# Optimization experiments

Measured on AMD Instinct MI355X. Metric: run time of the kernel, lower is better.

## Reference

```python
import jax, jax.numpy as jnp
import numpy as np

E = 256   # embed_dim
H = 8     # num_heads
D = E // H  # head_dim = 32
L = 1024  # seq len (Q_len == K_len == V_len)


def setup_inputs() -> dict:
    key = jax.random.key(0)
    ks = jax.random.split(key, 10)
    f = lambda k, s: jax.random.normal(k, s, dtype=jnp.float32)
    return {
        "V": f(ks[0], (L, E)),
        "K": f(ks[1], (L, E)),
        "Q": f(ks[2], (L, E)),
        # genomic-style coordinates, strictly positive
        "position": jax.random.uniform(ks[3], (L,), dtype=jnp.float32) * 1e5,
        "Wq": f(ks[4], (E, E)) * 0.02,
        "Wk": f(ks[5], (E, E)) * 0.02,
        "Wv": f(ks[6], (E, E)) * 0.02,
        "Wr": f(ks[7], (E, 1)) * 0.02,   # K_relative_linear weight [out=E, in=1]
        "Wo": f(ks[8], (E, E)) * 0.02,
        "bo": jnp.zeros((E,), jnp.float32),
    }


def reference(V, K, Q, position, Wq, Wk, Wv, Wr, Wo, bo):
    Lq = Q.shape[0]
    # projections (nn.Linear: x @ W.T), split into heads -> (L, H, D)
    q = (Q @ Wq.T).reshape(Lq, H, D)
    k = (K @ Wk.T).reshape(Lq, H, D)
    v = (V @ Wv.T).reshape(Lq, H, D)

    # relative position scalar per (q, k) pair: log(|p_q - p_k| + 1)
    rel = jnp.log(jnp.abs(position[:, None] - position[None, :]) + 1.0)  # (L, L)

    # K_relative_linear maps scalar rel -> (H, D); the einsum
    # 'nqhd,nhqjd->nhqj' then factorizes exactly as:
    #   sum_d Q[q,h,d] * rel[q,j] * Wr[h,d] = (Q . Wr)[h,q] * rel[q,j]
    # so we avoid materializing the (H, L, L, D) tensor while computing
    # mathematically identical results.
    Wr_h = Wr[:, 0].reshape(H, D)                    # (H, D)
    coeff = jnp.einsum('qhd,hd->hq', q, Wr_h)        # (H, L)

    energy = jnp.einsum('qhd,khd->hqk', q, k)        # (H, L, L)
    energy = energy + coeff[:, :, None] * rel[None, :, :]

    attn = jax.nn.softmax(energy / np.float32(E) ** 0.5, axis=2)
    out = jnp.einsum('hqk,khd->qhd', attn, v).reshape(Lq, E)
    out = out @ Wo.T + bo
    return out
```

## Files before the change

### kernel.cpp

```cpp
#include <hip/hip_runtime.h>
#include <math.h>

#define EDIM 256
#define LDIM 1024
#define HDIM 8
#define DDIM 32

typedef __attribute__((ext_vector_type(8))) short short8;
typedef __attribute__((ext_vector_type(4))) float f32x4;

__device__ inline unsigned short bf16h(float x) {
    unsigned u = __float_as_uint(x);
    return (unsigned short)((u + 0x7fff + ((u >> 16) & 1)) >> 16);
}
__device__ inline float bf16tof(unsigned short h) {
    return __uint_as_float(((unsigned)h) << 16);
}
__device__ inline float exp2fast(float x) {
    float r; asm volatile("v_exp_f32 %0, %1" : "=v"(r) : "v"(x)); return r;
}
__device__ inline float log2fast(float x) {
    float r; asm volatile("v_log_f32 %0, %1" : "=v"(r) : "v"(x)); return r;
}

#define SC2 0.09016843880556021f

__global__ __launch_bounds__(256) void proj_kernel(
    const float* __restrict__ Q, const float* __restrict__ Km, const float* __restrict__ V,
    const float* __restrict__ Wq, const float* __restrict__ Wk, const float* __restrict__ Wv,
    const float* __restrict__ Wr, const float* __restrict__ Wo,
    short* __restrict__ qThi, short* __restrict__ qTlo,
    short* __restrict__ kThi, short* __restrict__ kTlo,
    short* __restrict__ vThi, short* __restrict__ vTlo,
    float* __restrict__ coeff, short* __restrict__ Wohi, short* __restrict__ Wolo)
{
    const int z = blockIdx.z;
    const int tid = threadIdx.x;

    if (z == 3) {
        const int idx = ((blockIdx.y * 32 + blockIdx.x) << 8) + tid;
        const float w = Wo[idx];
        const unsigned short hh = bf16h(w);
        Wohi[idx] = (short)hh;
        Wolo[idx] = (short)bf16h(w - bf16tof(hh));
        return;
    }

    const float* __restrict__ X = (z == 0) ? Q : (z == 1) ? Km : V;
    const float* __restrict__ W = (z == 0) ? Wq : (z == 1) ? Wk : Wv;
    short* __restrict__ dhi     = (z == 0) ? qThi : (z == 1) ? kThi : vThi;
    short* __restrict__ dlo     = (z == 0) ? qTlo : (z == 1) ? kTlo : vTlo;

    const int n0 = blockIdx.x * 32;
    const int o0 = blockIdx.y * 32;
    const int wave = tid >> 6, lane = tid & 63;
    const int n = lane & 15, quad = lane >> 4;
    const int rh = wave & 1, oh = wave >> 1;

    const int s    = tid >> 7;
    const int r    = (tid >> 2) & 31;
    const int qd   = tid & 3;
    const int half = r >> 4;
    const int fl8  = ((r & 15) | (qd << 4)) * 8;

    __shared__ short Xhi[2][2][512], Xlo[2][2][512];
    __shared__ short Whi[2][2][512], Wlo[2][2][512];
    __shared__ float cpart[2][2][16];

    const float* xp = X + (n0 + r) * EDIM + s * 32 + qd * 8;
    const float* wp = W + (o0 + r) * EDIM + s * 32 + qd * 8;

    float4 xa0 = *(const float4*)xp, xa1 = *(const float4*)(xp + 4);
    float4 wa0 = *(const float4*)wp, wa1 = *(const float4*)(wp + 4);

    f32x4 acc = {0.f, 0.f, 0.f, 0.f};

    for (int kb = 0; kb < EDIM; kb += 64) {
        __syncthreads();
        {
            float xv[8] = {xa0.x,xa0.y,xa0.z,xa0.w, xa1.x,xa1.y,xa1.z,xa1.w};
            float wv[8] = {wa0.x,wa0.y,wa0.z,wa0.w, wa1.x,wa1.y,wa1.z,wa1.w};
            short8 xh, xl, wh, wl;
            #pragma unroll
            for (int j = 0; j < 8; ++j) {
                unsigned short xhh = bf16h(xv[j]);
                unsigned short whh = bf16h(wv[j]);
                xh[j] = (short)xhh; xl[j] = (short)bf16h(xv[j] - bf16tof(xhh));
                wh[j] = (short)whh; wl[j] = (short)bf16h(wv[j] - bf16tof(whh));
            }
            *(short8*)&Xhi[s][half][fl8] = xh;
            *(short8*)&Xlo[s][half][fl8] = xl;
            *(short8*)&Whi[s][half][fl8] = wh;
            *(short8*)&Wlo[s][half][fl8] = wl;
        }
        float4 xn0, xn1, wn0, wn1;
        if (kb + 64 < EDIM) {
            xn0 = *(const float4*)(xp + kb + 64); xn1 = *(const float4*)(xp + kb + 68);
            wn0 = *(const float4*)(wp + kb + 64); wn1 = *(const float4*)(wp + kb + 68);
        }
        __syncthreads();
        #pragma unroll
        for (int ss = 0; ss < 2; ++ss) {
            short8 ah = *(const short8*)&Xhi[ss][rh][lane*8];
            short8 al = *(const short8*)&Xlo[ss][rh][lane*8];
            short8 bh = *(const short8*)&Whi[ss][oh][lane*8];
            short8 bl = *(const short8*)&Wlo[ss][oh][lane*8];
            acc = __builtin_amdgcn_mfma_f32_16x16x32_bf16(al, bh, acc, 0, 0, 0);
            acc = __builtin_amdgcn_mfma_f32_16x16x32_bf16(ah, bl, acc, 0, 0, 0);
            acc = __builtin_amdgcn_mfma_f32_16x16x32_bf16(ah, bh, acc, 0, 0, 0);
        }
        xa0 = xn0; xa1 = xn1; wa0 = wn0; wa1 = wn1;
    }

    const int h  = o0 >> 5;
    const int og = oh * 16 + n;
    #pragma unroll
    for (int i = 0; i < 4; ++i) {
        const int row = rh * 16 + 4 * quad + i;
        const unsigned short hh = bf16h(acc[i]);
        dhi[(h * LDIM + n0 + row) * DDIM + og] = (short)hh;
        dlo[(h * LDIM + n0 + row) * DDIM + og] = (short)bf16h(acc[i] - bf16tof(hh));
    }

    if (z == 0) {
        const float wr = Wr[o0 + og];
        #pragma unroll
        for (int i = 0; i < 4; ++i) {
            float c = acc[i] * wr;
            c += __shfl_xor(c, 1, 64);
            c += __shfl_xor(c, 2, 64);
            c += __shfl_xor(c, 4, 64);
            c += __shfl_xor(c, 8, 64);
            if (n == 0) cpart[rh][oh][4*quad + i] = c;
        }
        __syncthreads();
        if (tid < 32)
            coeff[h * LDIM + n0 + tid] = cpart[tid >> 4][0][tid & 15]
                                       + cpart[tid >> 4][1][tid & 15];
    }
}

__global__ __launch_bounds__(256, 4) void attn_kernel(
    const short* __restrict__ qThi, const short* __restrict__ qTlo,
    const short* __restrict__ kThi, const short* __restrict__ kTlo,
    const short* __restrict__ vThi, const short* __restrict__ vTlo,
    const float* __restrict__ coeff, const float* __restrict__ pos,
    float* __restrict__ Op, float* __restrict__ Mp, float* __restrict__ Lp, int nkt)
{
    const int h   = blockIdx.y;
    const int q0  = blockIdx.x * 64;
    const int p   = blockIdx.z;
    const int kt0 = p * nkt * 64;
    const int tid  = threadIdx.x;
    const int wave = tid >> 6;
    const int lane = tid & 63;
    const int n    = lane & 15;
    const int quad = lane >> 4;
    const int qs0  = wave * 16;

    __shared__ __align__(16) short khi[4*64*8];
    __shared__ __align__(16) short klo[4*64*8];
    __shared__ __align__(16) short vs_hi[32][72];
    __shared__ __align__(16) short vs_lo[32][72];
    __shared__ __align__(16) short pa_hi[64][72];
    __shared__ __align__(16) short pa_lo[64][72];
    __shared__ float pk[64];

    const short8 qhi = *(const short8*)(qThi + (h*LDIM + q0 + qs0 + n) * DDIM + quad*8);
    const short8 qlo = *(const short8*)(qTlo + (h*LDIM + q0 + qs0 + n) * DDIM + quad*8);

    float pq[4], cq[4];
    #pragma unroll
    for (int i = 0; i < 4; ++i) {
        const int r = q0 + qs0 + 4*quad + i;
        pq[i] = pos[r];
        cq[i] = coeff[h*LDIM + r] * 0.0625f;
    }

    float m[4], l[4];
    #pragma unroll
    for (int i = 0; i < 4; ++i) { m[i] = -INFINITY; l[i] = 0.f; }

    f32x4 of0 = {0.f,0.f,0.f,0.f}, of1 = {0.f,0.f,0.f,0.f};

    const int cS = tid >> 2;
    const int dq = tid & 3;
    const int lane2 = (cS & 15) | (dq << 4);
    const int gS = cS >> 4;

    short8 khi_c, klo_c, vhi_c, vlo_c; float pkc = 0.f;
    {
        const int off = (h*LDIM + kt0 + cS) * DDIM + dq*8;
        khi_c = *(const short8*)(kThi + off);
        klo_c = *(const short8*)(kTlo + off);
        vhi_c = *(const short8*)(vThi + off);
        vlo_c = *(const short8*)(vTlo + off);
        if (tid < 64) pkc = pos[kt0 + tid];
    }

    for (int t = 0; t < nkt; ++t) {
        __syncthreads();

        *((short8*)&khi[(gS*64 + lane2)*8]) = khi_c;
        *((short8*)&klo[(gS*64 + lane2)*8]) = klo_c;
        #pragma unroll
        for (int j = 0; j < 8; ++j) {
            vs_hi[dq*8 + j][cS] = vhi_c[j];
            vs_lo[dq*8 + j][cS] = vlo_c[j];
        }
        if (tid < 64) pk[tid] = pkc;

        short8 khi_n, klo_n, vhi_n, vlo_n; float pkn = 0.f;
        if (t + 1 < nkt) {
            const int off = (h*LDIM + kt0 + (t+1)*64 + cS) * DDIM + dq*8;
            khi_n = *(const short8*)(kThi + off);
            klo_n = *(const short8*)(kTlo + off);
            vhi_n = *(const short8*)(vThi + off);
            vlo_n = *(const short8*)(vTlo + off);
            if (tid < 64) pkn = pos[kt0 + (t+1)*64 + tid];
        }
        __syncthreads();

        f32x4 Sf[4];
        #pragma unroll
        for (int t4 = 0; t4 < 4; ++t4) {
            short8 bhi = *((const short8*)&khi[(t4*64 + lane)*8]);
            short8 blo = *((const short8*)&klo[(t4*64 + lane)*8]);
            f32x4 acc = {0.f, 0.f, 0.f, 0.f};
            acc = __builtin_amdgcn_mfma_f32_16x16x32_bf16(qlo, bhi, acc, 0, 0, 0);
            acc = __builtin_amdgcn_mfma_f32_16x16x32_bf16(qhi, blo, acc, 0, 0, 0);
            acc = __builtin_amdgcn_mfma_f32_16x16x32_bf16(qhi, bhi, acc, 0, 0, 0);
            Sf[t4] = acc;
        }

        float ev[4][4];
        float rmax[4] = {-INFINITY, -INFINITY, -INFINITY, -INFINITY};
        #pragma unroll
        for (int t4 = 0; t4 < 4; ++t4) {
            const float pkt = pk[16*t4 + n];
            #pragma unroll
            for (int i = 0; i < 4; ++i) {
                float s = fmaf(Sf[t4][i], SC2, cq[i] * log2fast(fabsf(pq[i] - pkt) + 1.f));
                ev[t4][i] = s;
                rmax[i] = fmaxf(rmax[i], s);
            }
        }
        #pragma unroll
        for (int off = 1; off < 16; off <<= 1)
            #pragma unroll
            for (int i = 0; i < 4; ++i)
                rmax[i] = fmaxf(rmax[i], __shfl_xor(rmax[i], off, 64));

        float al[4], rsum[4];
        #pragma unroll
        for (int i = 0; i < 4; ++i) {
            const float mn = fmaxf(m[i], rmax[i]);
            al[i] = exp2fast(m[i] - mn);
            m[i] = mn;
            rsum[i] = 0.f;
        }
        #pragma unroll
        for (int t4 = 0; t4 < 4; ++t4)
            #pragma unroll
            for (int i = 0; i < 4; ++i) {
                float e = exp2fast(ev[t4][i] - m[i]);
                rsum[i] += e;
                unsigned u = __float_as_uint(e);
                pa_hi[qs0 + 4*quad + i][16*t4 + n] = (short)(u >> 16);
                float r = e - __uint_as_float(u & 0xffff0000u);
                pa_lo[qs0 + 4*quad + i][16*t4 + n] = (short)bf16h(r);
            }
        #pragma unroll
        for (int off = 1; off < 16; off <<= 1)
            #pragma unroll
            for (int i = 0; i < 4; ++i)
                rsum[i] += __shfl_xor(rsum[i], off, 64);
        #pragma unroll
        for (int i = 0; i < 4; ++i) l[i] = l[i]*al[i] + rsum[i];

        #pragma unroll
        for (int i = 0; i < 4; ++i) { of0[i] *= al[i]; of1[i] *= al[i]; }

        #pragma unroll
        for (int ch = 0; ch < 2; ++ch) {
            short8 phi = *(const short8*)&pa_hi[qs0 + n][ch*32 + quad*8];
            short8 plo = *(const short8*)&pa_lo[qs0 + n][ch*32 + quad*8];
            #pragma unroll
            for (int dt = 0; dt < 2; ++dt) {
                short8 vh8 = *(const short8*)&vs_hi[dt*16 + n][ch*32 + quad*8];
                short8 vl8 = *(const short8*)&vs_lo[dt*16 + n][ch*32 + quad*8];
                f32x4& of = dt ? of1 : of0;
                of = __builtin_amdgcn_mfma_f32_16x16x32_bf16(plo, vh8, of, 0, 0, 0);
                of = __builtin_amdgcn_mfma_f32_16x16x32_bf16(phi, vl8, of, 0, 0, 0);
                of = __builtin_amdgcn_mfma_f32_16x16x32_bf16(phi, vh8, of, 0, 0, 0);
            }
        }

        khi_c = khi_n; klo_c = klo_n; vhi_c = vhi_n; vlo_c = vlo_n; pkc = pkn;
    }

    const int ph = p * HDIM + h;
    {
        const size_t base = ((size_t)ph * LDIM + q0 + qs0) * DDIM;
        #pragma unroll
        for (int i = 0; i < 4; ++i) {
            Op[base + (size_t)(4*quad + i)*DDIM + n]      = of0[i];
            Op[base + (size_t)(4*quad + i)*DDIM + 16 + n] = of1[i];
        }
    }
    if (n == 0) {
        #pragma unroll
        for (int i = 0; i < 4; ++i) {
            const int r = q0 + qs0 + 4*quad + i;
            Mp[ph*LDIM + r] = m[i];
            Lp[ph*LDIM + r] = l[i];
        }
    }
}

__global__ __launch_bounds__(256) void finale_kernel(
    const float* __restrict__ Op, const float* __restrict__ Mp, const float* __restrict__ Lp,
    const short* __restrict__ Wohi, const short* __restrict__ Wolo,
    const float* __restrict__ bo, int P, float* __restrict__ out)
{
    const int n0 = blockIdx.x * 8;
    const int tid = threadIdx.x;

    __shared__ __align__(16) short Ahi[8][264], Alo[8][264];

    {
        const int r  = tid >> 5;
        const int c8 = (tid & 31) * 8;
        const int hh = c8 >> 5;
        const int d  = c8 & 31;
        float mv[8], lv[8];
        float mx = -INFINITY;
        #pragma unroll
        for (int p = 0; p < 8; ++p) if (p < P) {
            mv[p] = Mp[(p*HDIM + hh)*LDIM + n0 + r];
            lv[p] = Lp[(p*HDIM + hh)*LDIM + n0 + r];
            mx = fmaxf(mx, mv[p]);
        }
        float s = 0.f;
        #pragma unroll
        for (int p = 0; p < 8; ++p) if (p < P) {
            float a = exp2fast(mv[p] - mx);
            mv[p] = a;
            s += a * lv[p];
        }
        const float inv = 1.f / s;
        float a[8] = {0.f,0.f,0.f,0.f,0.f,0.f,0.f,0.f};
        #pragma unroll
        for (int p = 0; p < 8; ++p) if (p < P) {
            const float sp = mv[p] * inv;
            const float* op = Op + ((size_t)(p*HDIM + hh)*LDIM + n0 + r)*DDIM + d;
            float4 x0 = *(const float4*)op;
            float4 x1 = *(const float4*)(op + 4);
            a[0] += sp*x0.x; a[1] += sp*x0.y; a[2] += sp*x0.z; a[3] += sp*x0.w;
            a[4] += sp*x1.x; a[5] += sp*x1.y; a[6] += sp*x1.z; a[7] += sp*x1.w;
        }
        short8 ah8, al8;
        #pragma unroll
        for (int j = 0; j < 8; ++j) {
            const unsigned short hhh = bf16h(a[j]);
            ah8[j] = (short)hhh;
            al8[j] = (short)bf16h(a[j] - bf16tof(hhh));
        }
        *(short8*)&Ahi[r][c8] = ah8;
        *(short8*)&Alo[r][c8] = al8;
    }
    __syncthreads();

    const int wave = tid >> 6, lane = tid & 63;
    const int n = lane & 15, quad = lane >> 4;
    const int ow = wave * 64;
    const int rA = n & 7;

    f32x4 acc[4];
    #pragma unroll
    for (int cf = 0; cf < 4; ++cf) { acc[cf][0]=0.f; acc[cf][1]=0.f; acc[cf][2]=0.f; acc[cf][3]=0.f; }

    #pragma unroll
    for (int kk = 0; kk < 8; ++kk) {
        short8 ah = *(const short8*)&Ahi[rA][kk*32 + quad*8];
        short8 al = *(const short8*)&Alo[rA][kk*32 + quad*8];
        #pragma unroll
        for (int cf = 0; cf < 4; ++cf) {
            const int o = ow + cf*16 + n;
            short8 bh = *(const short8*)(Wohi + o*EDIM + kk*32 + quad*8);
            short8 bl = *(const short8*)(Wolo + o*EDIM + kk*32 + quad*8);
            acc[cf] = __builtin_amdgcn_mfma_f32_16x16x32_bf16(al, bh, acc[cf], 0, 0, 0);
            acc[cf] = __builtin_amdgcn_mfma_f32_16x16x32_bf16(ah, bl, acc[cf], 0, 0, 0);
            acc[cf] = __builtin_amdgcn_mfma_f32_16x16x32_bf16(ah, bh, acc[cf], 0, 0, 0);
        }
    }

    if (quad < 2) {
        #pragma unroll
        for (int cf = 0; cf < 4; ++cf) {
            const int o = ow + cf*16 + n;
            const float b = bo[o];
            #pragma unroll
            for (int i = 0; i < 4; ++i) {
                const int row = n0 + 4*quad + i;
                out[row*EDIM + o] = acc[cf][i] + b;
            }
        }
    }
}

extern "C" void kernel_launch(void* const* d_in, const int* in_sizes, int n_in,
                              void* d_out, int out_size, void* d_ws, size_t ws_size,
                              hipStream_t stream) {
    const float* V   = (const float*)d_in[0];
    const float* K   = (const float*)d_in[1];
    const float* Q   = (const float*)d_in[2];
    const float* pos = (const float*)d_in[3];
    const float* Wq  = (const float*)d_in[4];
    const float* Wk  = (const float*)d_in[5];
    const float* Wv  = (const float*)d_in[6];
    const float* Wr  = (const float*)d_in[7];
    const float* Wo  = (const float*)d_in[8];
    const float* bo  = (const float*)d_in[9];
    float* out = (float*)d_out;
    char* base = (char*)d_ws;

    auto need = [](int P) -> size_t { return 3440640 + (size_t)P * 1114112; };
    int P = 2;
    if (ws_size >= need(8)) P = 8;
    else if (ws_size >= need(4)) P = 4;

    short* qThi  = (short*)(base);
    short* qTlo  = (short*)(base + 524288);
    short* kThi  = (short*)(base + 1048576);
    short* kTlo  = (short*)(base + 1572864);
    short* vThi  = (short*)(base + 2097152);
    short* vTlo  = (short*)(base + 2621440);
    float* coeff = (float*)(base + 3145728);
    short* Wohi  = (short*)(base + 3178496);
    short* Wolo  = (short*)(base + 3309568);
    float* Op    = (float*)(base + 3440640);
    float* Mp    = Op + (size_t)P * 262144;
    float* Lp    = Mp + (size_t)P * 8192;

    proj_kernel  <<<dim3(32, 8, 4), 256, 0, stream>>>(Q, K, V, Wq, Wk, Wv, Wr, Wo,
                                                      qThi, qTlo, kThi, kTlo, vThi, vTlo,
                                                      coeff, Wohi, Wolo);
    attn_kernel  <<<dim3(16, 8, P), 256, 0, stream>>>(qThi, qTlo, kThi, kTlo, vThi, vTlo,
                                                      coeff, pos, Op, Mp, Lp, 16 / P);
    finale_kernel<<<dim3(128),      256, 0, stream>>>(Op, Mp, Lp, Wohi, Wolo, bo, P, out);
}
```

Measured before the change: 109.8 us.

## Split finale into combine kernel and LDS-tiled double-buffered output projection

The fused finale kernel, which merged split-K attention partials and ran the Wo projection with Wo fragments read straight from global memory, is split into two kernels. A combine kernel merges the partials and writes hi/lo bf16 activations into the now-free q buffers. A separate 32x32-tiled out-projection kernel stages activation and weight tiles through LDS, prefetching the next k-slice into registers. This improves Wo reuse and raises grid size from 128 to 256 blocks, at the cost of an extra kernel launch and a global round trip for the combined activations.

```diff
diff --git a/kernel.cpp b/kernel.cpp
--- a/kernel.cpp
+++ b/kernel.cpp
@@ -7,6 +7,7 @@
 #define DDIM 32
 
 typedef __attribute__((ext_vector_type(8))) short short8;
+typedef __attribute__((ext_vector_type(4))) short shortx4;
 typedef __attribute__((ext_vector_type(4))) float f32x4;
 
 __device__ inline unsigned short bf16h(float x) {
@@ -318,94 +319,118 @@
     }
 }
 
-__global__ __launch_bounds__(256) void finale_kernel(
+__global__ __launch_bounds__(256) void combine_kernel(
     const float* __restrict__ Op, const float* __restrict__ Mp, const float* __restrict__ Lp,
+    int P, short* __restrict__ Ahi, short* __restrict__ Alo)
+{
+    const int idx = blockIdx.x * 256 + threadIdx.x;
+    const int n  = idx >> 6;
+    const int e4 = (idx & 63) * 4;
+    const int h  = e4 >> 5;
+    const int d  = e4 & 31;
+
+    float mv[8], lv[8];
+    float mx = -INFINITY;
+    #pragma unroll
+    for (int p = 0; p < 8; ++p) if (p < P) {
+        mv[p] = Mp[(p*HDIM + h)*LDIM + n];
+        lv[p] = Lp[(p*HDIM + h)*LDIM + n];
+        mx = fmaxf(mx, mv[p]);
+    }
+    float s = 0.f;
+    #pragma unroll
+    for (int p = 0; p < 8; ++p) if (p < P) {
+        float a = exp2fast(mv[p] - mx);
+        mv[p] = a;
+        s += a * lv[p];
+    }
+    const float inv = 1.f / s;
+
+    float4 x; x.x = x.y = x.z = x.w = 0.f;
+    #pragma unroll
+    for (int p = 0; p < 8; ++p) if (p < P) {
+        const float sp = mv[p] * inv;
+        float4 xp = *(const float4*)(Op + ((size_t)(p*HDIM + h)*LDIM + n)*DDIM + d);
+        x.x += sp*xp.x; x.y += sp*xp.y; x.z += sp*xp.z; x.w += sp*xp.w;
+    }
+    float a4[4] = {x.x, x.y, x.z, x.w};
+    shortx4 ah4, al4;
+    #pragma unroll
+    for (int j = 0; j < 4; ++j) {
+        const unsigned short hh = bf16h(a4[j]);
+        ah4[j] = (short)hh;
+        al4[j] = (short)bf16h(a4[j] - bf16tof(hh));
+    }
+    *(shortx4*)(Ahi + n*EDIM + e4) = ah4;
+    *(shortx4*)(Alo + n*EDIM + e4) = al4;
+}
+
+__global__ __launch_bounds__(256) void outproj_kernel(
+    const short* __restrict__ Ahi, const short* __restrict__ Alo,
     const short* __restrict__ Wohi, const short* __restrict__ Wolo,
-    const float* __restrict__ bo, int P, float* __restrict__ out)
+    const float* __restrict__ bo, float* __restrict__ out)
 {
-    const int n0 = blockIdx.x * 8;
+    const int n0 = blockIdx.x * 32;
+    const int o0 = blockIdx.y * 32;
     const int tid = threadIdx.x;
-
-    __shared__ __align__(16) short Ahi[8][264], Alo[8][264];
-
-    {
-        const int r  = tid >> 5;
-        const int c8 = (tid & 31) * 8;
-        const int hh = c8 >> 5;
-        const int d  = c8 & 31;
-        float mv[8], lv[8];
-        float mx = -INFINITY;
-        #pragma unroll
-        for (int p = 0; p < 8; ++p) if (p < P) {
-            mv[p] = Mp[(p*HDIM + hh)*LDIM + n0 + r];
-            lv[p] = Lp[(p*HDIM + hh)*LDIM + n0 + r];
-            mx = fmaxf(mx, mv[p]);
-        }
-        float s = 0.f;
-        #pragma unroll
-        for (int p = 0; p < 8; ++p) if (p < P) {
-            float a = exp2fast(mv[p] - mx);
-            mv[p] = a;
-            s += a * lv[p];
-        }
-        const float inv = 1.f / s;
-        float a[8] = {0.f,0.f,0.f,0.f,0.f,0.f,0.f,0.f};
-        #pragma unroll
-        for (int p = 0; p < 8; ++p) if (p < P) {
-            const float sp = mv[p] * inv;
-            const float* op = Op + ((size_t)(p*HDIM + hh)*LDIM + n0 + r)*DDIM + d;
-            float4 x0 = *(const float4*)op;
-            float4 x1 = *(const float4*)(op + 4);
-            a[0] += sp*x0.x; a[1] += sp*x0.y; a[2] += sp*x0.z; a[3] += sp*x0.w;
-            a[4] += sp*x1.x; a[5] += sp*x1.y; a[6] += sp*x1.z; a[7] += sp*x1.w;
-        }
-        short8 ah8, al8;
-        #pragma unroll
-        for (int j = 0; j < 8; ++j) {
-            const unsigned short hhh = bf16h(a[j]);
-            ah8[j] = (short)hhh;
-            al8[j] = (short)bf16h(a[j] - bf16tof(hhh));
-        }
-        *(short8*)&Ahi[r][c8] = ah8;
-        *(short8*)&Alo[r][c8] = al8;
-    }
-    __syncthreads();
-
     const int wave = tid >> 6, lane = tid & 63;
     const int n = lane & 15, quad = lane >> 4;
-    const int ow = wave * 64;
-    const int rA = n & 7;
-
-    f32x4 acc[4];
-    #pragma unroll
-    for (int cf = 0; cf < 4; ++cf) { acc[cf][0]=0.f; acc[cf][1]=0.f; acc[cf][2]=0.f; acc[cf][3]=0.f; }
-
-    #pragma unroll
-    for (int kk = 0; kk < 8; ++kk) {
-        short8 ah = *(const short8*)&Ahi[rA][kk*32 + quad*8];
-        short8 al = *(const short8*)&Alo[rA][kk*32 + quad*8];
-        #pragma unroll
-        for (int cf = 0; cf < 4; ++cf) {
-            const int o = ow + cf*16 + n;
-            short8 bh = *(const short8*)(Wohi + o*EDIM + kk*32 + quad*8);
-            short8 bl = *(const short8*)(Wolo + o*EDIM + kk*32 + quad*8);
-            acc[cf] = __builtin_amdgcn_mfma_f32_16x16x32_bf16(al, bh, acc[cf], 0, 0, 0);
-            acc[cf] = __builtin_amdgcn_mfma_f32_16x16x32_bf16(ah, bl, acc[cf], 0, 0, 0);
-            acc[cf] = __builtin_amdgcn_mfma_f32_16x16x32_bf16(ah, bh, acc[cf], 0, 0, 0);
-        }
-    }
-
-    if (quad < 2) {
-        #pragma unroll
-        for (int cf = 0; cf < 4; ++cf) {
-            const int o = ow + cf*16 + n;
-            const float b = bo[o];
-            #pragma unroll
-            for (int i = 0; i < 4; ++i) {
-                const int row = n0 + 4*quad + i;
-                out[row*EDIM + o] = acc[cf][i] + b;
-            }
-        }
+    const int rh = wave & 1, oh = wave >> 1;
+
+    const int s    = tid >> 7;
+    const int r    = (tid >> 2) & 31;
+    const int qd   = tid & 3;
+    const int half = r >> 4;
+    const int fl8  = ((r & 15) | (qd << 4)) * 8;
+
+    __shared__ short Xhi[2][2][512], Xlo[2][2][512];
+    __shared__ short Whi[2][2][512], Wlo[2][2][512];
+
+    const short* xph = Ahi  + (n0 + r) * EDIM + s * 32 + qd * 8;
+    const short* xpl = Alo  + (n0 + r) * EDIM + s * 32 + qd * 8;
+    const short* wph = Wohi + (o0 + r) * EDIM + s * 32 + qd * 8;
+    const short* wpl = Wolo + (o0 + r) * EDIM + s * 32 + qd * 8;
+
+    short8 xh_c = *(const short8*)xph;
+    short8 xl_c = *(const short8*)xpl;
+    short8 wh_c = *(const short8*)wph;
+    short8 wl_c = *(const short8*)wpl;
+
+    f32x4 acc = {0.f, 0.f, 0.f, 0.f};
+
+    for (int kb = 0; kb < EDIM; kb += 64) {
+        __syncthreads();
+        *(short8*)&Xhi[s][half][fl8] = xh_c;
+        *(short8*)&Xlo[s][half][fl8] = xl_c;
+        *(short8*)&Whi[s][half][fl8] = wh_c;
+        *(short8*)&Wlo[s][half][fl8] = wl_c;
+        short8 xh_n, xl_n, wh_n, wl_n;
+        if (kb + 64 < EDIM) {
+            xh_n = *(const short8*)(xph + kb + 64);
+            xl_n = *(const short8*)(xpl + kb + 64);
+            wh_n = *(const short8*)(wph + kb + 64);
+            wl_n = *(const short8*)(wpl + kb + 64);
+        }
+        __syncthreads();
+        #pragma unroll
+        for (int ss = 0; ss < 2; ++ss) {
+            short8 ah = *(const short8*)&Xhi[ss][rh][lane*8];
+            short8 al = *(const short8*)&Xlo[ss][rh][lane*8];
+            short8 bh = *(const short8*)&Whi[ss][oh][lane*8];
+            short8 bl = *(const short8*)&Wlo[ss][oh][lane*8];
+            acc = __builtin_amdgcn_mfma_f32_16x16x32_bf16(al, bh, acc, 0, 0, 0);
+            acc = __builtin_amdgcn_mfma_f32_16x16x32_bf16(ah, bl, acc, 0, 0, 0);
+            acc = __builtin_amdgcn_mfma_f32_16x16x32_bf16(ah, bh, acc, 0, 0, 0);
+        }
+        xh_c = xh_n; xl_c = xl_n; wh_c = wh_n; wl_c = wl_n;
+    }
+
+    const int og = o0 + oh*16 + n;
+    const float b = bo[og];
+    #pragma unroll
+    for (int i = 0; i < 4; ++i) {
+        const int row = n0 + rh*16 + 4*quad + i;
+        out[row * EDIM + og] = acc[i] + b;
     }
 }
 
@@ -442,11 +467,14 @@
     float* Op    = (float*)(base + 3440640);
     float* Mp    = Op + (size_t)P * 262144;
     float* Lp    = Mp + (size_t)P * 8192;
-
-    proj_kernel  <<<dim3(32, 8, 4), 256, 0, stream>>>(Q, K, V, Wq, Wk, Wv, Wr, Wo,
-                                                      qThi, qTlo, kThi, kTlo, vThi, vTlo,
-                                                      coeff, Wohi, Wolo);
-    attn_kernel  <<<dim3(16, 8, P), 256, 0, stream>>>(qThi, qTlo, kThi, kTlo, vThi, vTlo,
-                                                      coeff, pos, Op, Mp, Lp, 16 / P);
-    finale_kernel<<<dim3(128),      256, 0, stream>>>(Op, Mp, Lp, Wohi, Wolo, bo, P, out);
-}
+    short* Ahi   = qThi;
+    short* Alo   = qTlo;
+
+    proj_kernel   <<<dim3(32, 8, 4), 256, 0, stream>>>(Q, K, V, Wq, Wk, Wv, Wr, Wo,
+                                                       qThi, qTlo, kThi, kTlo, vThi, vTlo,
+                                                       coeff, Wohi, Wolo);
+    attn_kernel   <<<dim3(16, 8, P), 256, 0, stream>>>(qThi, qTlo, kThi, kTlo, vThi, vTlo,
+                                                       coeff, pos, Op, Mp, Lp, 16 / P);
+    combine_kernel<<<dim3(256),      256, 0, stream>>>(Op, Mp, Lp, P, Ahi, Alo);
+    outproj_kernel<<<dim3(32, 8),    256, 0, stream>>>(Ahi, Alo, Wohi, Wolo, bo, out);
+}
```

After: 104.6 us. 1.05x faster.
